# Performance work log

Measured on AMD Instinct MI355X. Metric: run time of the kernel, lower is better.

## Reference

```python
import jax, jax.numpy as jnp
import numpy as np

N, H, T, E, L = 10000, 512, 4, 40000, 2
TIMESTEPS = (2, 2)  # layer_timesteps


def setup_inputs() -> dict:
    key = jax.random.key(0)
    ks = jax.random.split(key, 10)
    s = 1.0 / np.sqrt(H)
    u = lambda k, shape: jax.random.uniform(k, shape, jnp.float32, -s, s)
    return {
        "x": jax.random.normal(ks[0], (N, H), jnp.float32),
        "edges": jax.random.randint(ks[1], (T, E, 2), 0, N),  # (src, tgt)
        "W_msg": u(ks[2], (L, T, H, H)),   # torch Linear weight [out, in]
        "b_msg": u(ks[3], (L, T, H)),
        "W_ih": u(ks[4], (L, 3 * H, H)),   # GRUCell input weights (r,z,n)
        "W_hh": u(ks[5], (L, 3 * H, H)),
        "b_ih": u(ks[6], (L, 3 * H)),
        "b_hh": u(ks[7], (L, 3 * H)),
        "fc_W": u(ks[8], (H, H)),
        "fc_b": u(ks[9], (H,)),
    }


def _gru_cell(x, h, W_ih, W_hh, b_ih, b_hh):
    # torch.nn.GRUCell math
    gi = x @ W_ih.T + b_ih  # [N, 3H]
    gh = h @ W_hh.T + b_hh
    i_r, i_z, i_n = jnp.split(gi, 3, axis=-1)
    h_r, h_z, h_n = jnp.split(gh, 3, axis=-1)
    r = jax.nn.sigmoid(i_r + h_r)
    z = jax.nn.sigmoid(i_z + h_z)
    n = jnp.tanh(i_n + r * h_n)
    return (1.0 - z) * n + z * h


def reference(x, edges, W_msg, b_msg, W_ih, W_hh, b_ih, b_hh, fc_W, fc_b):
    # dropout layers run in eval mode (identity)
    targets = edges[:, :, 1].reshape(-1)  # [T*E], concat order matches torch loop
    sources = edges[:, :, 0]              # [T, E]
    h = x
    for layer in range(L):
        for _ in range(TIMESTEPS[layer]):
            src_states = h[sources]  # [T, E, H] gather
            # per-edge-type Linear: y = x @ W.T + b
            msgs = jnp.einsum('teh,tkh->tek', src_states, W_msg[layer]) \
                   + b_msg[layer][:, None, :]
            incoming = jax.ops.segment_sum(msgs.reshape(-1, H), targets,
                                           num_segments=N)  # scatter_add
            h = _gru_cell(incoming, h, W_ih[layer], W_hh[layer],
                          b_ih[layer], b_hh[layer])
    out = h @ fc_W.T + fc_b          # [N, H]
    graph_repr = jnp.max(out, axis=0)  # max-pool over nodes -> [H]
    return graph_repr
```

## Files before the change

### kernel.cpp

```cpp
#include <hip/hip_runtime.h>
#include <hip/hip_bf16.h>


#define NN 10000
#define HD 512
#define NT 4
#define NE 40000
#define CAP 24
#define GYROWS 80

typedef __bf16 bf16x8 __attribute__((ext_vector_type(8)));
typedef float f32x4 __attribute__((ext_vector_type(4)));
union V16 { int4 i; bf16x8 b; };

typedef __attribute__((address_space(1))) const unsigned int gu32;
typedef __attribute__((address_space(3))) unsigned int lu32;
__device__ __forceinline__ void gll16(const void* g, void* l) {
    __builtin_amdgcn_global_load_lds((gu32*)g, (lu32*)l, 16, 0, 0);
}

__device__ __forceinline__ float bfl(__bf16 v) { return (float)v; }

__device__ __forceinline__ int4 cvt8(const float* __restrict__ s) {
    float4 v0 = *(const float4*)s, v1 = *(const float4*)(s + 4);
    V16 o;
    o.b[0] = (__bf16)v0.x; o.b[1] = (__bf16)v0.y; o.b[2] = (__bf16)v0.z; o.b[3] = (__bf16)v0.w;
    o.b[4] = (__bf16)v1.x; o.b[5] = (__bf16)v1.y; o.b[6] = (__bf16)v1.z; o.b[7] = (__bf16)v1.w;
    return o.i;
}

__device__ __forceinline__ void pk_decode(int rem, int KTbits, int& col, int& kk) {
    int ct = rem >> (KTbits + 9);
    int r2 = rem & ((1 << (KTbits + 9)) - 1);
    int kt = r2 >> 9, s = r2 & 511;
    int lane = s & 63;
    col = ct * 128 + ((s >> 8) << 6) + (((s >> 6) & 3) << 4) + (lane & 15);
    kk = kt * 32 + ((lane >> 4) & 3) * 8;
}

__global__ void prep_all(const float* __restrict__ Wmsg, const float* __restrict__ Wih,
                         const float* __restrict__ Whh, const float* __restrict__ fcW,
                         const float* __restrict__ x, const int* __restrict__ edges,
                         int4* __restrict__ WmPK, int4* __restrict__ WrznhPK,
                         int4* __restrict__ WfPK,
                         __hip_bfloat16* __restrict__ ab,
                         int* __restrict__ bcnt, int* __restrict__ bins) {
    int blk = blockIdx.x, tid = threadIdx.x;
    if (blk < 1024) {
        int g = blk * 256 + tid;
        int l = g >> 17, rem = g & 131071;
        int col, kk; pk_decode(rem, 4, col, kk);
        WmPK[g] = cvt8(Wmsg + (size_t)l * 1048576 + (size_t)col * 512 + kk);
        return;
    }
    blk -= 1024;
    if (blk < 2048) {
        int g = blk * 256 + tid;
        int l = g >> 18, rem = g & 262143;
        int col, kk; pk_decode(rem, 5, col, kk);
        int gate = (col >> 4) & 3;
        int hcol = ((col >> 7) * 2 + ((col >> 6) & 1)) * 16 + (col & 15);
        int4 v = make_int4(0, 0, 0, 0);
        if (kk < 512) {
            if (gate < 3) v = cvt8(Wih + (size_t)l * 786432 + (size_t)(gate * 512 + hcol) * 512 + kk);
        } else {
            if (gate < 2) v = cvt8(Whh + (size_t)l * 786432 + (size_t)(gate * 512 + hcol) * 512 + (kk - 512));
            else if (gate == 3) v = cvt8(Whh + (size_t)l * 786432 + (size_t)(1024 + hcol) * 512 + (kk - 512));
        }
        WrznhPK[g] = v;
        return;
    }
    blk -= 2048;
    if (blk < 128) {
        int g = blk * 256 + tid;
        int col, kk; pk_decode(g, 4, col, kk);
        WfPK[g] = cvt8(fcW + (size_t)col * 512 + kk);
        return;
    }
    blk -= 128;
    if (blk < 5000) {
        int i = blk * 1024 + tid * 4;
        float4 v = *(const float4*)(x + i);
        int m = i >> 9, c = i & 511;
        __hip_bfloat16 o[4] = {__float2bfloat16(v.x), __float2bfloat16(v.y),
                               __float2bfloat16(v.z), __float2bfloat16(v.w)};
        *(ulong1*)(ab + (size_t)m * 1024 + 512 + c) = *(ulong1*)o;
        return;
    }
    blk -= 5000;
    {
        int i = blk * 256 + tid;
        if (i >= NT * NE) return;
        int src = edges[2 * i], tgt = edges[2 * i + 1];
        int t = i / NE;
        int b = tgt * NT + t;
        int pos = atomicAdd(&bcnt[b], 1);
        if (pos < CAP) bins[(size_t)b * CAP + pos] = src;
    }
}

__global__ __launch_bounds__(256) void gather_msum(
    const int* __restrict__ bins, const int* __restrict__ bcnt,
    const float* __restrict__ bm, const __hip_bfloat16* __restrict__ Msg,
    __hip_bfloat16* __restrict__ inc) {
    int wave = threadIdx.x >> 6, lane = threadIdx.x & 63;
    int n = blockIdx.x * 4 + wave;
    int co = lane * 8;
    float acc[8] = {0, 0, 0, 0, 0, 0, 0, 0};
#pragma unroll
    for (int t = 0; t < NT; ++t) {
        int bi = n * NT + t;
        int cnt = bcnt[bi]; if (cnt > CAP) cnt = CAP;
        const int* bl = bins + (size_t)bi * CAP;
        for (int e = 0; e < cnt; ++e) {
            int src = bl[e];
            V16 v; v.i = *(const int4*)(Msg + (size_t)src * 2048 + t * 512 + co);
#pragma unroll
            for (int k = 0; k < 8; ++k) acc[k] += (float)v.b[k];
        }
        float4 b0 = *(const float4*)(bm + t * 512 + co);
        float4 b1 = *(const float4*)(bm + t * 512 + co + 4);
        float fc = (float)cnt;
        acc[0] += fc * b0.x; acc[1] += fc * b0.y; acc[2] += fc * b0.z; acc[3] += fc * b0.w;
        acc[4] += fc * b1.x; acc[5] += fc * b1.y; acc[6] += fc * b1.z; acc[7] += fc * b1.w;
    }
    V16 o;
#pragma unroll
    for (int k = 0; k < 8; ++k) o.b[k] = (__bf16)acc[k];
    *(int4*)(inc + (size_t)n * 1024 + co) = o.i;
}

__device__ __forceinline__ unsigned fenc(float f) {
    unsigned b = __float_as_uint(f);
    return b ^ (((int)b >> 31) | 0x80000000u);
}
__device__ __forceinline__ float fdec(unsigned u) {
    unsigned b = (u & 0x80000000u) ? (u ^ 0x80000000u) : ~u;
    return __uint_as_float(b);
}

template<int MODE>
__global__ __launch_bounds__(256) void gemm(
    const __hip_bfloat16* __restrict__ A, int lda, int K,
    const int4* __restrict__ Wpk,
    const float* __restrict__ b0, const float* __restrict__ b1,
    __hip_bfloat16* __restrict__ obf, int ldo,
    unsigned* __restrict__ om) {
    __shared__ int4 sA4[3][1024];
    __shared__ unsigned sm[128];
    __hip_bfloat16* lds = (__hip_bfloat16*)sA4;
    float2* ldsZ = (float2*)sA4;

    const int NB = (MODE == 3) ? 4 : 16;
    int bid = blockIdx.x;
    int xcd = bid & 7, kq = bid >> 3;
    int bcol = kq % NB;
    int brow = xcd + 8 * (kq / NB);
    int m0 = brow * 128, n0 = bcol * 128;

    int tid = threadIdx.x;
    int lane = tid & 63, wave = tid >> 6;
    int wr = wave >> 1, wc = wave & 1;
    int lm = lane & 15, quad = lane >> 4;
    int qx = (lm >> 1) & 3;

    const int KT32 = K >> 5;
    const int KT = K >> 6;
    const int kend = KT;
    const int4* Wp = Wpk + ((size_t)bcol * KT32 << 9) + wc * 256 + lane;

    auto issueA = [&](int kt, int p) {
        int k0 = kt << 6;
#pragma unroll
        for (int it = 0; it < 4; ++it) {
            int idx = it * 256 + tid;
            int s = idx >> 9, rem = idx & 511;
            int row = rem >> 2;
            int kc = (rem & 3) ^ ((row >> 1) & 3);
            int gm = m0 + row; gm = gm < NN ? gm : NN - 1;
            gll16(A + (size_t)gm * lda + k0 + s * 32 + kc * 8,
                  (__hip_bfloat16*)(sA4[p]) + idx * 8);
        }
    };
    auto loadB = [&](int kt, int4 (&bb)[2][4]) {
#pragma unroll
        for (int s = 0; s < 2; ++s) {
            const int4* wn = Wp + ((size_t)(2 * kt + s) << 9);
#pragma unroll
            for (int j = 0; j < 4; ++j) bb[s][j] = wn[j * 64];
        }
    };

    f32x4 acc[4][4] = {};
    int4 bb0[2][4], bb1[2][4];
    issueA(0, 0);
    issueA(1, 1);
    loadB(0, bb0);

    auto ktbody = [&](int kt, int4 (&bbCur)[2][4], int4 (&bbNxt)[2][4]) {
        int p = kt % 3;
        if (kt + 1 < kend) loadB(kt + 1, bbNxt);
        __builtin_amdgcn_sched_barrier(0);
        if (kt + 1 < kend) __builtin_amdgcn_s_waitcnt(0x4F74);
        else               __builtin_amdgcn_s_waitcnt(0x0F78);
        __builtin_amdgcn_s_barrier();
        __builtin_amdgcn_sched_barrier(0);
        V16 a[4][2];
#pragma unroll
        for (int i = 0; i < 4; ++i)
#pragma unroll
            for (int s = 0; s < 2; ++s)
                a[i][s].i = sA4[p][s * 512 + (wr * 64 + i * 16 + lm) * 4 + (quad ^ qx)];
        if (kt + 2 < kend) issueA(kt + 2, (kt + 2) % 3);
#pragma unroll
        for (int s = 0; s < 2; ++s)
#pragma unroll
            for (int i = 0; i < 4; ++i)
#pragma unroll
                for (int j = 0; j < 4; ++j) {
                    if (MODE == 1) {
                        if (j == 2 && kt >= 8) continue;
                        if (j == 3 && kt < 8) continue;
                    }
                    V16 b; b.i = bbCur[s][j];
                    acc[i][j] = __builtin_amdgcn_mfma_f32_16x16x32_bf16(a[i][s].b, b.b, acc[i][j], 0, 0, 0);
                }
        __builtin_amdgcn_sched_barrier(0);
    };

    for (int k2 = 0; k2 < kend; k2 += 2) {
        ktbody(k2, bb0, bb1);
        ktbody(k2 + 1, bb1, bb0);
    }

    if (MODE == 0) {
        __syncthreads();
#pragma unroll
        for (int ph = 0; ph < 2; ++ph) {
            if (wr == ph) {
#pragma unroll
                for (int j = 0; j < 4; ++j) {
                    int c = wc * 64 + j * 16 + lm;
#pragma unroll
                    for (int i = 0; i < 4; ++i)
#pragma unroll
                        for (int r = 0; r < 4; ++r)
                            lds[(i * 16 + quad * 4 + r) * 128 + c] = __float2bfloat16(acc[i][j][r]);
                }
            }
            __syncthreads();
#pragma unroll
            for (int q = 0; q < 4; ++q) {
                int idx = q * 256 + tid;
                int rl = idx >> 4, c16 = idx & 15;
                int m = m0 + ph * 64 + rl;
                if (m < NN)
                    *(int4*)(obf + (size_t)m * ldo + n0 + c16 * 8) =
                        *(const int4*)(lds + rl * 128 + c16 * 8);
            }
            __syncthreads();
        }
    } else if (MODE == 1) {
        __syncthreads();
        int c32 = wc * 16 + lm;
        int hcol = bcol * 32 + c32;
        float rb = b0[hcol] + b1[hcol];
        float zb = b0[512 + hcol] + b1[512 + hcol];
        float ib = b0[1024 + hcol];
        float hb = b1[1024 + hcol];
#pragma unroll
        for (int i = 0; i < 4; ++i)
#pragma unroll
            for (int r = 0; r < 4; ++r) {
                int rloc = wr * 64 + i * 16 + quad * 4 + r;
                float rr = 1.f / (1.f + __expf(-(acc[i][0][r] + rb)));
                float zz = 1.f / (1.f + __expf(-(acc[i][1][r] + zb)));
                float nx = (acc[i][2][r] + ib) + rr * (acc[i][3][r] + hb);
                float n = 1.f - 2.f / (__expf(2.f * nx) + 1.f);
                ldsZ[rloc * 34 + c32] = make_float2((1.f - zz) * n, zz);
            }
        __syncthreads();
#pragma unroll
        for (int q = 0; q < 4; ++q) {
            int idx = q * 256 + tid;
            int rl = idx >> 3, c4 = (idx & 7) * 4;
            int m = m0 + rl;
            if (m < NN) {
                ulong1 hraw = *(const ulong1*)(A + (size_t)m * lda + 512 + bcol * 32 + c4);
                const __bf16* hb4 = (const __bf16*)&hraw;
                const float2* pz = ldsZ + rl * 34 + c4;
                __hip_bfloat16 ob[4];
#pragma unroll
                for (int e = 0; e < 4; ++e) {
                    float2 az = pz[e];
                    ob[e] = __float2bfloat16(az.x + az.y * bfl(hb4[e]));
                }
                *(ulong1*)(obf + (size_t)m * ldo + bcol * 32 + c4) = *(ulong1*)ob;
            }
        }
    } else {
        if (tid < 128) sm[tid] = 0;
        __syncthreads();
#pragma unroll
        for (int j = 0; j < 4; ++j) {
            int c = wc * 64 + j * 16 + lm;
            float bias = b0[n0 + c];
            float mx = -INFINITY;
#pragma unroll
            for (int i = 0; i < 4; ++i) {
                int r0 = m0 + wr * 64 + i * 16 + quad * 4;
#pragma unroll
                for (int r = 0; r < 4; ++r) {
                    int m = r0 + r;
                    if (m < NN) mx = fmaxf(mx, acc[i][j][r] + bias);
                }
            }
            atomicMax(&sm[c], fenc(mx));
        }
        __syncthreads();
        if (tid < 128) atomicMax(&om[n0 + tid], sm[tid]);
    }
}

__global__ void writeout(const unsigned* __restrict__ om, float* __restrict__ o) {
    int c = threadIdx.x;
    o[c] = fdec(om[c]);
}

extern "C" void kernel_launch(void* const* d_in, const int* in_sizes, int n_in,
                              void* d_out, int out_size, void* d_ws, size_t ws_size,
                              hipStream_t stream) {
    (void)in_sizes; (void)n_in; (void)out_size; (void)ws_size;
    const float* x    = (const float*)d_in[0];
    const int*   edges= (const int*)d_in[1];
    const float* Wmsg = (const float*)d_in[2];
    const float* bmsg = (const float*)d_in[3];
    const float* Wih  = (const float*)d_in[4];
    const float* Whh  = (const float*)d_in[5];
    const float* bih  = (const float*)d_in[6];
    const float* bhh  = (const float*)d_in[7];
    const float* fcW  = (const float*)d_in[8];
    const float* fcb  = (const float*)d_in[9];
    float* out = (float*)d_out;

    char* ws = (char*)d_ws;
    size_t off = 0;
    auto alloc = [&](size_t bytes) -> void* {
        void* p = ws + off; off += (bytes + 255) & ~(size_t)255; return p;
    };
    __hip_bfloat16* abA  = (__hip_bfloat16*)alloc((size_t)NN * 1024 * 2);
    __hip_bfloat16* abB  = (__hip_bfloat16*)alloc((size_t)NN * 1024 * 2);
    int*            bcnt = (int*)alloc((size_t)NN * NT * 4);
    int*            bins = (int*)alloc((size_t)NN * NT * CAP * 4);
    unsigned*       om   = (unsigned*)alloc(HD * 4);
    int4*           WmPK   = (int4*)alloc((size_t)2 * 131072 * 16);
    int4*           WrznhPK= (int4*)alloc((size_t)2 * 262144 * 16);
    int4*           WfPK   = (int4*)alloc((size_t)32768 * 16);
    __hip_bfloat16* Msg  = (__hip_bfloat16*)alloc((size_t)NN * 2048 * 2);

    hipMemsetAsync(bcnt, 0, (size_t)NN * NT * 4, stream);
    hipMemsetAsync(om, 0, HD * 4, stream);
    prep_all<<<1024 + 2048 + 128 + 5000 + 625, 256, 0, stream>>>(
        Wmsg, Wih, Whh, fcW, x, edges, WmPK, WrznhPK, WfPK, abA, bcnt, bins);

    for (int s = 0; s < 4; ++s) {
        int layer = s >> 1;
        __hip_bfloat16* cur = (s & 1) ? abB : abA;
        __hip_bfloat16* nxt = (s & 1) ? abA : abB;
        const int4* Wm = WmPK + (size_t)layer * 131072;
        const int4* Wz = WrznhPK + (size_t)layer * 262144;
        const float* bm = bmsg + (size_t)layer * 2048;
        const float* bi = bih + (size_t)layer * 1536;
        const float* bh = bhh + (size_t)layer * 1536;

        gemm<0><<<16 * GYROWS, 256, 0, stream>>>(cur + 512, 1024, 512, Wm,
            nullptr, nullptr, Msg, 2048, nullptr);
        gather_msum<<<NN / 4, 256, 0, stream>>>(bins, bcnt, bm, Msg, cur);
        gemm<1><<<16 * GYROWS, 256, 0, stream>>>(cur, 1024, 1024, Wz,
            bi, bh, nxt + 512, 1024, nullptr);
    }
    gemm<3><<<4 * GYROWS, 256, 0, stream>>>(abA + 512, 1024, 512, WfPK,
        fcb, nullptr, nullptr, 0, om);
    writeout<<<1, 512, 0, stream>>>(om, out);
}
```

Baseline: 574.1 us.

## Switch GEMM to single-wave 64x64 tiles with double-buffered LDS

Restructures the bf16 MFMA GEMM from 256-thread blocks computing 128x128 tiles to 64-thread single-wave blocks computing 64x64 tiles. The grid grows fourfold, A staging drops from a triple to a double buffer, and the workgroup barrier in the k-loop is replaced by an LDS-only waitcnt. The aim is higher occupancy and less barrier overhead with more blocks. In exchange, each block reuses A and B data less, which raises global and L2 traffic per flop.

```diff
diff --git a/kernel.cpp b/kernel.cpp
--- a/kernel.cpp
+++ b/kernel.cpp
@@ -7,7 +7,7 @@
 #define NT 4
 #define NE 40000
 #define CAP 24
-#define GYROWS 80
+#define GR 160
 
 typedef __bf16 bf16x8 __attribute__((ext_vector_type(8)));
 typedef float f32x4 __attribute__((ext_vector_type(4)));
@@ -140,41 +140,40 @@
 }
 
 template<int MODE>
-__global__ __launch_bounds__(256) void gemm(
+__global__ __launch_bounds__(64) void gemm(
     const __hip_bfloat16* __restrict__ A, int lda, int K,
     const int4* __restrict__ Wpk,
     const float* __restrict__ b0, const float* __restrict__ b1,
     __hip_bfloat16* __restrict__ obf, int ldo,
     unsigned* __restrict__ om) {
-    __shared__ int4 sA4[3][1024];
-    __shared__ unsigned sm[128];
-    __hip_bfloat16* lds = (__hip_bfloat16*)sA4;
+    __shared__ int4 sA4[2][512];
+    __shared__ unsigned sm[64];
+    __hip_bfloat16* lt = (__hip_bfloat16*)sA4;
     float2* ldsZ = (float2*)sA4;
 
-    const int NB = (MODE == 3) ? 4 : 16;
+    const int NBC = (MODE == 3) ? 8 : 32;
     int bid = blockIdx.x;
     int xcd = bid & 7, kq = bid >> 3;
-    int bcol = kq % NB;
-    int brow = xcd + 8 * (kq / NB);
-    int m0 = brow * 128, n0 = bcol * 128;
-
-    int tid = threadIdx.x;
-    int lane = tid & 63, wave = tid >> 6;
-    int wr = wave >> 1, wc = wave & 1;
+    int bcol = kq % NBC;
+    int brow = xcd + 8 * (kq / NBC);
+    int m0 = brow * 64, n0 = bcol * 64;
+
+    int lane = threadIdx.x;
     int lm = lane & 15, quad = lane >> 4;
     int qx = (lm >> 1) & 3;
 
     const int KT32 = K >> 5;
     const int KT = K >> 6;
     const int kend = KT;
-    const int4* Wp = Wpk + ((size_t)bcol * KT32 << 9) + wc * 256 + lane;
+    int ct = bcol >> 1, wcc = bcol & 1;
+    const int4* Wp = Wpk + ((size_t)ct * KT32 << 9) + wcc * 256 + lane;
 
     auto issueA = [&](int kt, int p) {
         int k0 = kt << 6;
 #pragma unroll
-        for (int it = 0; it < 4; ++it) {
-            int idx = it * 256 + tid;
-            int s = idx >> 9, rem = idx & 511;
+        for (int it = 0; it < 8; ++it) {
+            int idx = it * 64 + lane;
+            int s = idx >> 8, rem = idx & 255;
             int row = rem >> 2;
             int kc = (rem & 3) ^ ((row >> 1) & 3);
             int gm = m0 + row; gm = gm < NN ? gm : NN - 1;
@@ -198,20 +197,21 @@
     loadB(0, bb0);
 
     auto ktbody = [&](int kt, int4 (&bbCur)[2][4], int4 (&bbNxt)[2][4]) {
-        int p = kt % 3;
+        int p = kt & 1;
         if (kt + 1 < kend) loadB(kt + 1, bbNxt);
         __builtin_amdgcn_sched_barrier(0);
-        if (kt + 1 < kend) __builtin_amdgcn_s_waitcnt(0x4F74);
+        if (kt + 1 < kend) __builtin_amdgcn_s_waitcnt(0x4F78);
         else               __builtin_amdgcn_s_waitcnt(0x0F78);
-        __builtin_amdgcn_s_barrier();
         __builtin_amdgcn_sched_barrier(0);
         V16 a[4][2];
 #pragma unroll
         for (int i = 0; i < 4; ++i)
 #pragma unroll
             for (int s = 0; s < 2; ++s)
-                a[i][s].i = sA4[p][s * 512 + (wr * 64 + i * 16 + lm) * 4 + (quad ^ qx)];
-        if (kt + 2 < kend) issueA(kt + 2, (kt + 2) % 3);
+                a[i][s].i = sA4[p][s * 256 + (i * 16 + lm) * 4 + (quad ^ qx)];
+        __builtin_amdgcn_s_waitcnt(0xC07F);
+        __builtin_amdgcn_sched_barrier(0);
+        if (kt + 2 < kend) issueA(kt + 2, p);
 #pragma unroll
         for (int s = 0; s < 2; ++s)
 #pragma unroll
@@ -236,34 +236,25 @@
     if (MODE == 0) {
         __syncthreads();
 #pragma unroll
-        for (int ph = 0; ph < 2; ++ph) {
-            if (wr == ph) {
-#pragma unroll
-                for (int j = 0; j < 4; ++j) {
-                    int c = wc * 64 + j * 16 + lm;
-#pragma unroll
-                    for (int i = 0; i < 4; ++i)
-#pragma unroll
-                        for (int r = 0; r < 4; ++r)
-                            lds[(i * 16 + quad * 4 + r) * 128 + c] = __float2bfloat16(acc[i][j][r]);
-                }
-            }
-            __syncthreads();
-#pragma unroll
-            for (int q = 0; q < 4; ++q) {
-                int idx = q * 256 + tid;
-                int rl = idx >> 4, c16 = idx & 15;
-                int m = m0 + ph * 64 + rl;
-                if (m < NN)
-                    *(int4*)(obf + (size_t)m * ldo + n0 + c16 * 8) =
-                        *(const int4*)(lds + rl * 128 + c16 * 8);
-            }
-            __syncthreads();
+        for (int j = 0; j < 4; ++j)
+#pragma unroll
+            for (int i = 0; i < 4; ++i)
+#pragma unroll
+                for (int r = 0; r < 4; ++r)
+                    lt[(i * 16 + quad * 4 + r) * 72 + j * 16 + lm] = __float2bfloat16(acc[i][j][r]);
+        __syncthreads();
+#pragma unroll
+        for (int q = 0; q < 8; ++q) {
+            int idx = q * 64 + lane;
+            int rl = idx >> 3, c8 = (idx & 7) * 8;
+            int m = m0 + rl;
+            if (m < NN)
+                *(int4*)(obf + (size_t)m * ldo + n0 + c8) =
+                    *(const int4*)(lt + rl * 72 + c8);
         }
     } else if (MODE == 1) {
         __syncthreads();
-        int c32 = wc * 16 + lm;
-        int hcol = bcol * 32 + c32;
+        int hcol = bcol * 16 + lm;
         float rb = b0[hcol] + b1[hcol];
         float zb = b0[512 + hcol] + b1[512 + hcol];
         float ib = b0[1024 + hcol];
@@ -272,43 +263,43 @@
         for (int i = 0; i < 4; ++i)
 #pragma unroll
             for (int r = 0; r < 4; ++r) {
-                int rloc = wr * 64 + i * 16 + quad * 4 + r;
+                int rloc = i * 16 + quad * 4 + r;
                 float rr = 1.f / (1.f + __expf(-(acc[i][0][r] + rb)));
                 float zz = 1.f / (1.f + __expf(-(acc[i][1][r] + zb)));
                 float nx = (acc[i][2][r] + ib) + rr * (acc[i][3][r] + hb);
                 float n = 1.f - 2.f / (__expf(2.f * nx) + 1.f);
-                ldsZ[rloc * 34 + c32] = make_float2((1.f - zz) * n, zz);
+                ldsZ[rloc * 17 + lm] = make_float2((1.f - zz) * n, zz);
             }
         __syncthreads();
 #pragma unroll
         for (int q = 0; q < 4; ++q) {
-            int idx = q * 256 + tid;
-            int rl = idx >> 3, c4 = (idx & 7) * 4;
+            int idx = q * 64 + lane;
+            int rl = idx >> 2, c4 = (idx & 3) * 4;
             int m = m0 + rl;
             if (m < NN) {
-                ulong1 hraw = *(const ulong1*)(A + (size_t)m * lda + 512 + bcol * 32 + c4);
+                ulong1 hraw = *(const ulong1*)(A + (size_t)m * lda + 512 + bcol * 16 + c4);
                 const __bf16* hb4 = (const __bf16*)&hraw;
-                const float2* pz = ldsZ + rl * 34 + c4;
+                const float2* pz = ldsZ + rl * 17 + c4;
                 __hip_bfloat16 ob[4];
 #pragma unroll
                 for (int e = 0; e < 4; ++e) {
                     float2 az = pz[e];
                     ob[e] = __float2bfloat16(az.x + az.y * bfl(hb4[e]));
                 }
-                *(ulong1*)(obf + (size_t)m * ldo + bcol * 32 + c4) = *(ulong1*)ob;
+                *(ulong1*)(obf + (size_t)m * ldo + bcol * 16 + c4) = *(ulong1*)ob;
             }
         }
     } else {
-        if (tid < 128) sm[tid] = 0;
+        sm[lane] = 0;
         __syncthreads();
 #pragma unroll
         for (int j = 0; j < 4; ++j) {
-            int c = wc * 64 + j * 16 + lm;
+            int c = j * 16 + lm;
             float bias = b0[n0 + c];
             float mx = -INFINITY;
 #pragma unroll
             for (int i = 0; i < 4; ++i) {
-                int r0 = m0 + wr * 64 + i * 16 + quad * 4;
+                int r0 = m0 + i * 16 + quad * 4;
 #pragma unroll
                 for (int r = 0; r < 4; ++r) {
                     int m = r0 + r;
@@ -318,7 +309,7 @@
             atomicMax(&sm[c], fenc(mx));
         }
         __syncthreads();
-        if (tid < 128) atomicMax(&om[n0 + tid], sm[tid]);
+        atomicMax(&om[n0 + lane], sm[lane]);
     }
 }
 
@@ -373,13 +364,13 @@
         const float* bi = bih + (size_t)layer * 1536;
         const float* bh = bhh + (size_t)layer * 1536;
 
-        gemm<0><<<16 * GYROWS, 256, 0, stream>>>(cur + 512, 1024, 512, Wm,
+        gemm<0><<<32 * GR, 64, 0, stream>>>(cur + 512, 1024, 512, Wm,
             nullptr, nullptr, Msg, 2048, nullptr);
         gather_msum<<<NN / 4, 256, 0, stream>>>(bins, bcnt, bm, Msg, cur);
-        gemm<1><<<16 * GYROWS, 256, 0, stream>>>(cur, 1024, 1024, Wz,
+        gemm<1><<<32 * GR, 64, 0, stream>>>(cur, 1024, 1024, Wz,
             bi, bh, nxt + 512, 1024, nullptr);
     }
-    gemm<3><<<4 * GYROWS, 256, 0, stream>>>(abA + 512, 1024, 512, WfPK,
+    gemm<3><<<8 * GR, 64, 0, stream>>>(abA + 512, 1024, 512, WfPK,
         fcb, nullptr, nullptr, 0, om);
     writeout<<<1, 512, 0, stream>>>(om, out);
 }
```

Result: slower. 634.6 us (+10.5%).
